# Kernel optimization log

Hardware: AMD Instinct MI355X
Metric: run time of the kernel (lower is better)

The kernel has to match this reference:

```python
import jax, jax.numpy as jnp
import numpy as np

NUM_HEADS = 16
MASKED_BIAS = -10000.0


def setup_inputs() -> dict:
    key = jax.random.key(0)
    k1, k2, k3 = jax.random.split(key, 3)
    B, S, D = 4, 2048, 1024
    scale = 0.02
    return {
        "hidden_states": jax.random.normal(k1, (B, S, D), dtype=jnp.float32),
        "c_attn_w": jax.random.normal(k2, (D, 3 * D), dtype=jnp.float32) * scale,
        "c_attn_b": jnp.zeros((3 * D,), dtype=jnp.float32),
        "c_proj_w": jax.random.normal(k3, (D, D), dtype=jnp.float32) * scale,
        "c_proj_b": jnp.zeros((D,), dtype=jnp.float32),
    }


def reference(hidden_states, c_attn_w, c_attn_b, c_proj_w, c_proj_b):
    B, S, D = hidden_states.shape
    H = NUM_HEADS
    hd = D // H
    # qkv projection (HF Conv1D: x @ W + b)
    qkv = hidden_states @ c_attn_w + c_attn_b  # [B, S, 3D]
    q, k, v = jnp.split(qkv, 3, axis=-1)

    def split_heads(t):
        return t.reshape(B, S, H, hd).transpose(0, 2, 1, 3)  # [B, H, S, hd]

    q, k, v = split_heads(q), split_heads(k), split_heads(v)
    # full score matrix [B, H, S, S] (eager attention)
    attn = jnp.einsum("bhqd,bhkd->bhqk", q, k) / jnp.sqrt(jnp.float32(hd))
    causal = jnp.tril(jnp.ones((S, S), dtype=bool))  # [S, S]
    attn = jnp.where(causal[None, None], attn, jnp.float32(MASKED_BIAS))
    attn = jax.nn.softmax(attn, axis=-1)
    out = jnp.einsum("bhqk,bhkd->bhqd", attn, v)  # [B, H, S, hd]
    out = out.transpose(0, 2, 1, 3).reshape(B, S, D)  # merge heads
    out = out @ c_proj_w + c_proj_b
    return out
```

## Files before the change

kernel.cpp:

```cpp
#include <hip/hip_runtime.h>

#define NH 16
#define HD 64

typedef __attribute__((ext_vector_type(8))) _Float16 f16x8;
typedef __attribute__((ext_vector_type(4))) float f32x4;
typedef __attribute__((ext_vector_type(8))) unsigned short us8;
typedef __attribute__((ext_vector_type(4))) unsigned short us4;
typedef __attribute__((ext_vector_type(2))) unsigned int u32x2;

#define CEXP 0.18033688f

__device__ __forceinline__ unsigned short f2h(float f) {
    _Float16 h = (_Float16)f;
    return __builtin_bit_cast(unsigned short, h);
}

__global__ __launch_bounds__(256)
void transpose_cast_both(const float* __restrict__ w1, unsigned short* __restrict__ o1,
                         const float* __restrict__ w2, unsigned short* __restrict__ o2) {
    __shared__ float T[64][65];
    const int R = 1024;
    int bx = blockIdx.x;
    const float* in; unsigned short* out; int C;
    if (bx < 48) { in = w1; out = o1; C = 3072; }
    else         { in = w2; out = o2; C = 1024; bx -= 48; }
    const int c0 = bx * 64, r0 = blockIdx.y * 64;
    const int tid = threadIdx.x;
    const int rr = tid >> 4, cc4 = (tid & 15) * 4;
    #pragma unroll
    for (int p = 0; p < 4; ++p) {
        int r = rr + p * 16;
        float4 v = *reinterpret_cast<const float4*>(
            in + (size_t)(r0 + r) * C + c0 + cc4);
        T[r][cc4] = v.x; T[r][cc4 + 1] = v.y; T[r][cc4 + 2] = v.z; T[r][cc4 + 3] = v.w;
    }
    __syncthreads();
    #pragma unroll
    for (int p = 0; p < 4; ++p) {
        int orow = rr + p * 16;
        us4 w;
        #pragma unroll
        for (int j = 0; j < 4; ++j) w[j] = f2h(T[cc4 + j][orow]);
        *reinterpret_cast<us4*>(out + (size_t)(c0 + orow) * R + r0 + cc4) = w;
    }
}

__device__ __forceinline__ void stage128(unsigned short* dst,
                                         const unsigned short* src, int stride) {
    const int tid = threadIdx.x;
    #pragma unroll
    for (int p = 0; p < 4; ++p) {
        int idx = tid + p * 256;
        int r = idx >> 3;
        int slot = idx & 7;
        us8 v = *reinterpret_cast<const us8*>(src + (size_t)r * stride + slot * 8);
        int cb = (slot << 4) ^ ((r & 7) << 4);
        *reinterpret_cast<us8*>(reinterpret_cast<char*>(dst) + r * 128 + cb) = v;
    }
}

__device__ __forceinline__ void stage128_f32(unsigned short* dst,
                                             const float* src, int stride) {
    const int tid = threadIdx.x;
    #pragma unroll
    for (int p = 0; p < 4; ++p) {
        int idx = tid + p * 256;
        int r = idx >> 3;
        int slot = idx & 7;
        const float* s = src + (size_t)r * stride + slot * 8;
        float4 a = *reinterpret_cast<const float4*>(s);
        float4 b = *reinterpret_cast<const float4*>(s + 4);
        uint4 w;
        w.x = __builtin_bit_cast(unsigned int, __builtin_amdgcn_cvt_pkrtz(a.x, a.y));
        w.y = __builtin_bit_cast(unsigned int, __builtin_amdgcn_cvt_pkrtz(a.z, a.w));
        w.z = __builtin_bit_cast(unsigned int, __builtin_amdgcn_cvt_pkrtz(b.x, b.y));
        w.w = __builtin_bit_cast(unsigned int, __builtin_amdgcn_cvt_pkrtz(b.z, b.w));
        int cb = (slot << 4) ^ ((r & 7) << 4);
        *reinterpret_cast<uint4*>(reinterpret_cast<char*>(dst) + r * 128 + cb) = w;
    }
}

__device__ __forceinline__ void stage64(unsigned short* dst,
                                        const unsigned short* src, int stride) {
    const int tid = threadIdx.x;
    #pragma unroll
    for (int p = 0; p < 2; ++p) {
        int idx = tid + p * 256;
        int r = idx >> 3;
        int slot = idx & 7;
        us8 v = *reinterpret_cast<const us8*>(src + (size_t)r * stride + slot * 8);
        int cb = (slot << 4) ^ ((r & 7) << 4);
        *reinterpret_cast<us8*>(reinterpret_cast<char*>(dst) + r * 128 + cb) = v;
    }
}

__device__ __forceinline__ f16x8 frag16(const unsigned short* base, int row0, int ks) {
    const int lane = threadIdx.x & 63;
    const int r = row0 + (lane & 15);
    int cb = ((ks << 6) + (lane & 48)) ^ ((r & 7) << 4);
    return *reinterpret_cast<const f16x8*>(
        reinterpret_cast<const char*>(base) + r * 128 + cb);
}

template<int MODE, int NX>
__global__ __launch_bounds__(256)
void gemm_f16(const void* __restrict__ Ax,
              const unsigned short* __restrict__ Bt,
              const float* __restrict__ bias,
              float* __restrict__ C,
              unsigned short* __restrict__ qb,
              unsigned short* __restrict__ kb,
              unsigned short* __restrict__ vtb,
              int M, int N, int K) {
    __shared__ __align__(16) unsigned short As[128 * 64];
    __shared__ __align__(16) unsigned short Bs[128 * 64];

    const int tid = threadIdx.x;
    const int wid = tid >> 6, lane = tid & 63, g = lane >> 4;
    const int wr = wid >> 1, wc = wid & 1;

    const int f = blockIdx.x;
    const int wi = f >> 3;
    const int m0 = ((wi / NX) * 8 + (f & 7)) * 128;
    const int n0 = (wi % NX) * 128;

    f32x4 acc[4][4];
    #pragma unroll
    for (int i = 0; i < 4; ++i)
        #pragma unroll
        for (int j = 0; j < 4; ++j) {
            acc[i][j][0] = 0.f; acc[i][j][1] = 0.f;
            acc[i][j][2] = 0.f; acc[i][j][3] = 0.f;
        }

    for (int k0 = 0; k0 < K; k0 += 64) {
        __syncthreads();
        if (MODE == 1)
            stage128_f32(As, (const float*)Ax + (size_t)m0 * K + k0, K);
        else
            stage128(As, (const unsigned short*)Ax + (size_t)m0 * K + k0, K);
        stage128(Bs, Bt + (size_t)n0 * K + k0, K);
        __syncthreads();

        f16x8 af[4][2], bf[4][2];
        #pragma unroll
        for (int mi = 0; mi < 4; ++mi)
            #pragma unroll
            for (int ks = 0; ks < 2; ++ks)
                af[mi][ks] = frag16(As, wr * 64 + mi * 16, ks);
        #pragma unroll
        for (int ni = 0; ni < 4; ++ni)
            #pragma unroll
            for (int ks = 0; ks < 2; ++ks)
                bf[ni][ks] = frag16(Bs, wc * 64 + ni * 16, ks);

        __builtin_amdgcn_s_setprio(1);
        #pragma unroll
        for (int ks = 0; ks < 2; ++ks)
            #pragma unroll
            for (int mi = 0; mi < 4; ++mi)
                #pragma unroll
                for (int ni = 0; ni < 4; ++ni)
                    acc[mi][ni] = __builtin_amdgcn_mfma_f32_16x16x32_f16(
                        af[mi][ks], bf[ni][ks], acc[mi][ni], 0, 0, 0);
        __builtin_amdgcn_s_setprio(0);
    }

    const int colBase = n0 + wc * 64;
    const int rowBase = m0 + wr * 64;

    if (MODE == 0) {
        #pragma unroll
        for (int ni = 0; ni < 4; ++ni) {
            int col = colBase + ni * 16 + (lane & 15);
            float bv = bias[col];
            #pragma unroll
            for (int mi = 0; mi < 4; ++mi) {
                int row = rowBase + mi * 16 + g * 4;
                #pragma unroll
                for (int reg = 0; reg < 4; ++reg)
                    C[(size_t)(row + reg) * N + col] = acc[mi][ni][reg] + bv;
            }
        }
    } else {
        #pragma unroll
        for (int ni = 0; ni < 4; ++ni) {
            int col = colBase + ni * 16 + (lane & 15);
            float bv = bias[col];
            int seg = col >> 10;
            int cc = col & 1023;
            int h = cc >> 6, d = cc & 63;
            const float sc = (seg == 0) ? CEXP : 1.0f;
            #pragma unroll
            for (int mi = 0; mi < 4; ++mi) {
                int row = rowBase + mi * 16 + g * 4;
                int b = row >> 11, s = row & 2047;
                size_t bh = (size_t)(b * NH + h);
                if (seg < 2) {
                    unsigned short* dst = (seg ? kb : qb)
                        + bh * 2048 * 64 + (size_t)s * 64 + d;
                    #pragma unroll
                    for (int reg = 0; reg < 4; ++reg)
                        dst[(size_t)reg * 64] = f2h((acc[mi][ni][reg] + bv) * sc);
                } else {
                    unsigned short* dst = vtb
                        + bh * 64 * 2048 + (size_t)d * 2048 + s;
                    us4 w;
                    #pragma unroll
                    for (int reg = 0; reg < 4; ++reg)
                        w[reg] = f2h(acc[mi][ni][reg] + bv);
                    *reinterpret_cast<us4*>(dst) = w;
                }
            }
        }
    }
}

template<bool DIAG>
__device__ __forceinline__ void attn_tile(
    f16x8 qf0, f16x8 qf1,
    const unsigned short* Ks, const unsigned short* Vs, unsigned short* Pw,
    f32x4 (&o)[4], float& l_,
    int kt, int qrow_base, int lane, int g) {

    f32x4 s[4];
    #pragma unroll
    for (int n = 0; n < 4; ++n) { s[n][0] = 0.f; s[n][1] = 0.f; s[n][2] = 0.f; s[n][3] = 0.f; }

    __builtin_amdgcn_s_setprio(1);
    #pragma unroll
    for (int ks = 0; ks < 2; ++ks) {
        f16x8 b = ks ? qf1 : qf0;
        #pragma unroll
        for (int n = 0; n < 4; ++n)
            s[n] = __builtin_amdgcn_mfma_f32_16x16x32_f16(
                frag16(Ks, n * 16, ks), b, s[n], 0, 0, 0);
    }
    __builtin_amdgcn_s_setprio(0);

    const int q = lane & 15;
    float psum = 0.f;
    #pragma unroll
    for (int n = 0; n < 4; ++n) {
        float p0 = __builtin_exp2f(s[n][0]);
        float p1 = __builtin_exp2f(s[n][1]);
        float p2 = __builtin_exp2f(s[n][2]);
        float p3 = __builtin_exp2f(s[n][3]);
        if (DIAG) {
            const int kb_ = kt * 64 + (g << 2) + 16 * n;
            const int qg = qrow_base + q;
            p0 = (kb_ + 0 > qg) ? 0.f : p0;
            p1 = (kb_ + 1 > qg) ? 0.f : p1;
            p2 = (kb_ + 2 > qg) ? 0.f : p2;
            p3 = (kb_ + 3 > qg) ? 0.f : p3;
        }
        psum += (p0 + p1) + (p2 + p3);
        u32x2 w;
        w[0] = __builtin_bit_cast(unsigned int, __builtin_amdgcn_cvt_pkrtz(p0, p1));
        w[1] = __builtin_bit_cast(unsigned int, __builtin_amdgcn_cvt_pkrtz(p2, p3));
        int pcb = ((n << 5) + (g << 3)) ^ ((q & 7) << 4);
        *reinterpret_cast<u32x2*>(
            reinterpret_cast<char*>(Pw) + q * 128 + pcb) = w;
    }
    l_ += psum;

    __builtin_amdgcn_s_setprio(1);
    #pragma unroll
    for (int ks = 0; ks < 2; ++ks) {
        f16x8 pa = frag16(Pw, 0, ks);
        #pragma unroll
        for (int n = 0; n < 4; ++n)
            o[n] = __builtin_amdgcn_mfma_f32_16x16x32_f16(
                pa, frag16(Vs, n * 16, ks), o[n], 0, 0, 0);
    }
    __builtin_amdgcn_s_setprio(0);
}

__global__ __launch_bounds__(256, 4)
void attn_mfma(const unsigned short* __restrict__ qb,
               const unsigned short* __restrict__ kb,
               const unsigned short* __restrict__ vtb,
               unsigned short* __restrict__ attno) {
    const int f = blockIdx.x;
    const int xcd = f & 7;
    const int wi = f >> 3;
    const int bh = xcd * 8 + (wi >> 4);
    const int pair = wi & 15;
    const int qtA = pair, qtB = 31 - pair;
    const int tid = threadIdx.x;
    const int wid = tid >> 6, lane = tid & 63, g = lane >> 4;

    __shared__ __align__(16) unsigned short Ks[64 * 64];
    __shared__ __align__(16) unsigned short Vs[64 * 64];
    __shared__ __align__(16) unsigned short Ps[4][16 * 64];

    const unsigned short* kg0 = kb + (size_t)bh * 2048 * 64;
    const unsigned short* vg0 = vtb + (size_t)bh * 64 * 2048;

    const int qrl = wid * 16 + (lane & 15);
    const int qd0 = (lane >> 4) * 8;
    const unsigned short* qbase = qb + (size_t)bh * 2048 * 64;
    f16x8 qA0 = *reinterpret_cast<const f16x8*>(qbase + (size_t)(qtA * 64 + qrl) * 64 + qd0);
    f16x8 qA1 = *reinterpret_cast<const f16x8*>(qbase + (size_t)(qtA * 64 + qrl) * 64 + 32 + qd0);
    f16x8 qB0 = *reinterpret_cast<const f16x8*>(qbase + (size_t)(qtB * 64 + qrl) * 64 + qd0);
    f16x8 qB1 = *reinterpret_cast<const f16x8*>(qbase + (size_t)(qtB * 64 + qrl) * 64 + 32 + qd0);

    f32x4 oA[4], oB[4];
    float lA = 0.f, lB = 0.f;
    #pragma unroll
    for (int n = 0; n < 4; ++n) {
        #pragma unroll
        for (int r = 0; r < 4; ++r) { oA[n][r] = 0.f; oB[n][r] = 0.f; }
    }

    unsigned short* Pw = Ps[wid];
    const int qrbA = qtA * 64 + wid * 16;
    const int qrbB = qtB * 64 + wid * 16;

    auto STAGE = [&](int kt) {
        __syncthreads();
        stage64(Ks, kg0 + (size_t)kt * 64 * 64, 64);
        stage64(Vs, vg0 + (size_t)kt * 64, 2048);
        __syncthreads();
    };

    for (int kt = 0; kt < qtA; ++kt) {
        STAGE(kt);
        attn_tile<false>(qB0, qB1, Ks, Vs, Pw, oB, lB, kt, qrbB, lane, g);
        attn_tile<false>(qA0, qA1, Ks, Vs, Pw, oA, lA, kt, qrbA, lane, g);
    }
    STAGE(qtA);
    attn_tile<false>(qB0, qB1, Ks, Vs, Pw, oB, lB, qtA, qrbB, lane, g);
    attn_tile<true >(qA0, qA1, Ks, Vs, Pw, oA, lA, qtA, qrbA, lane, g);
    for (int kt = qtA + 1; kt < qtB; ++kt) {
        STAGE(kt);
        attn_tile<false>(qB0, qB1, Ks, Vs, Pw, oB, lB, kt, qrbB, lane, g);
    }
    STAGE(qtB);
    attn_tile<true >(qB0, qB1, Ks, Vs, Pw, oB, lB, qtB, qrbB, lane, g);

    const int b = bh >> 4, h = bh & 15;
    #pragma unroll
    for (int ph = 0; ph < 2; ++ph) {
        const int qt = ph ? qtB : qtA;
        f32x4* o = ph ? oB : oA;
        float ltot = ph ? lB : lA;
        ltot += __shfl_xor(ltot, 16);
        ltot += __shfl_xor(ltot, 32);
        unsigned short* ob = attno
            + (size_t)(b * 2048 + qt * 64 + wid * 16) * 1024 + h * 64;
        #pragma unroll
        for (int reg = 0; reg < 4; ++reg) {
            int row = (g << 2) + reg;
            float inv = 1.0f / __shfl(ltot, row);
            #pragma unroll
            for (int n = 0; n < 4; ++n)
                ob[(size_t)row * 1024 + n * 16 + (lane & 15)] = f2h(o[n][reg] * inv);
        }
    }
}

extern "C" void kernel_launch(void* const* d_in, const int* in_sizes, int n_in,
                              void* d_out, int out_size, void* d_ws, size_t ws_size,
                              hipStream_t stream) {
    const float* x    = (const float*)d_in[0];
    const float* Wqkv = (const float*)d_in[1];
    const float* bqkv = (const float*)d_in[2];
    const float* Wp   = (const float*)d_in[3];
    const float* bp   = (const float*)d_in[4];
    float* out = (float*)d_out;

    const int B = 4, S = 2048, D = 1024;
    const int M = B * S;
    const size_t HSZ = (size_t)M * D;

    unsigned short* wqt   = (unsigned short*)d_ws;
    unsigned short* wpt   = wqt + (size_t)3 * D * D;
    unsigned short* qbuf  = wpt + (size_t)D * D;
    unsigned short* kbuf  = qbuf + HSZ;
    unsigned short* vtb   = kbuf + HSZ;
    unsigned short* attno = vtb + HSZ;

    dim3 blk(256);
    transpose_cast_both<<<dim3(64, 16), blk, 0, stream>>>(Wqkv, wqt, Wp, wpt);

    gemm_f16<1, 24><<<dim3(1536), blk, 0, stream>>>(
        x, wqt, bqkv, nullptr, qbuf, kbuf, vtb, M, 3 * D, D);
    attn_mfma<<<dim3(1024), blk, 0, stream>>>(qbuf, kbuf, vtb, attno);
    gemm_f16<0, 8><<<dim3(512), blk, 0, stream>>>(
        attno, wpt, bp, out, nullptr, nullptr, nullptr, M, D, D);
}
```

Before: 173.8 us.

## Switch attention to 32x32x16 MFMA with 128-row query chunks per block

Reworks the attention kernel so each wave handles 32 query rows with 32x32x16 MFMA tiles instead of 16-row 16x16x32 tiles. Each block now processes two 128-row query chunks paired for causal load balance, halving the grid and the number of K/V stage loads per query row. The aim is to raise K/V reuse per shared-memory stage and MFMA efficiency. The cost is larger per-thread accumulators and lower occupancy (launch bound 2), plus more wasted work in the diagonal tiles.

```diff
diff --git a/kernel.cpp b/kernel.cpp
--- a/kernel.cpp
+++ b/kernel.cpp
@@ -5,6 +5,7 @@
 
 typedef __attribute__((ext_vector_type(8))) _Float16 f16x8;
 typedef __attribute__((ext_vector_type(4))) float f32x4;
+typedef __attribute__((ext_vector_type(16))) float f32x16;
 typedef __attribute__((ext_vector_type(8))) unsigned short us8;
 typedef __attribute__((ext_vector_type(4))) unsigned short us4;
 typedef __attribute__((ext_vector_type(2))) unsigned int u32x2;
@@ -99,6 +100,14 @@
     const int lane = threadIdx.x & 63;
     const int r = row0 + (lane & 15);
     int cb = ((ks << 6) + (lane & 48)) ^ ((r & 7) << 4);
+    return *reinterpret_cast<const f16x8*>(
+        reinterpret_cast<const char*>(base) + r * 128 + cb);
+}
+
+__device__ __forceinline__ f16x8 frag32(const unsigned short* base, int row0, int c) {
+    const int lane = threadIdx.x & 63;
+    const int r = row0 + (lane & 31);
+    int cb = ((c << 5) + ((lane >> 5) << 4)) ^ ((r & 7) << 4);
     return *reinterpret_cast<const f16x8*>(
         reinterpret_cast<const char*>(base) + r * 128 + cb);
 }
@@ -218,66 +227,69 @@
 }
 
 template<bool DIAG>
-__device__ __forceinline__ void attn_tile(
-    f16x8 qf0, f16x8 qf1,
+__device__ __forceinline__ void attn_slice(
+    const f16x8 (&qf)[4],
     const unsigned short* Ks, const unsigned short* Vs, unsigned short* Pw,
-    f32x4 (&o)[4], float& l_,
-    int kt, int qrow_base, int lane, int g) {
-
-    f32x4 s[4];
-    #pragma unroll
-    for (int n = 0; n < 4; ++n) { s[n][0] = 0.f; s[n][1] = 0.f; s[n][2] = 0.f; s[n][3] = 0.f; }
+    f32x16 (&o)[2], float& l_, int kt, int qsb, int lane) {
+
+    const int hf = lane >> 5;
+    const int q = lane & 31;
+
+    f32x16 s[2];
+    #pragma unroll
+    for (int n = 0; n < 2; ++n)
+        #pragma unroll
+        for (int r = 0; r < 16; ++r) s[n][r] = 0.f;
 
     __builtin_amdgcn_s_setprio(1);
     #pragma unroll
-    for (int ks = 0; ks < 2; ++ks) {
-        f16x8 b = ks ? qf1 : qf0;
-        #pragma unroll
-        for (int n = 0; n < 4; ++n)
-            s[n] = __builtin_amdgcn_mfma_f32_16x16x32_f16(
-                frag16(Ks, n * 16, ks), b, s[n], 0, 0, 0);
+    for (int c = 0; c < 4; ++c) {
+        #pragma unroll
+        for (int n = 0; n < 2; ++n)
+            s[n] = __builtin_amdgcn_mfma_f32_32x32x16_f16(
+                frag32(Ks, n * 32, c), qf[c], s[n], 0, 0, 0);
     }
     __builtin_amdgcn_s_setprio(0);
 
-    const int q = lane & 15;
+    const int qg = qsb + q;
     float psum = 0.f;
     #pragma unroll
-    for (int n = 0; n < 4; ++n) {
-        float p0 = __builtin_exp2f(s[n][0]);
-        float p1 = __builtin_exp2f(s[n][1]);
-        float p2 = __builtin_exp2f(s[n][2]);
-        float p3 = __builtin_exp2f(s[n][3]);
-        if (DIAG) {
-            const int kb_ = kt * 64 + (g << 2) + 16 * n;
-            const int qg = qrow_base + q;
-            p0 = (kb_ + 0 > qg) ? 0.f : p0;
-            p1 = (kb_ + 1 > qg) ? 0.f : p1;
-            p2 = (kb_ + 2 > qg) ? 0.f : p2;
-            p3 = (kb_ + 3 > qg) ? 0.f : p3;
+    for (int n = 0; n < 2; ++n) {
+        #pragma unroll
+        for (int j = 0; j < 4; ++j) {
+            float p[4];
+            #pragma unroll
+            for (int i = 0; i < 4; ++i) {
+                float v = __builtin_exp2f(s[n][j * 4 + i]);
+                if (DIAG) {
+                    int kg = kt * 64 + n * 32 + 8 * j + 4 * hf + i;
+                    if (kg > qg) v = 0.f;
+                }
+                p[i] = v; psum += v;
+            }
+            u32x2 w;
+            w[0] = __builtin_bit_cast(unsigned int, __builtin_amdgcn_cvt_pkrtz(p[0], p[1]));
+            w[1] = __builtin_bit_cast(unsigned int, __builtin_amdgcn_cvt_pkrtz(p[2], p[3]));
+            int pb = (n * 64 + j * 16 + hf * 8) ^ ((q & 7) << 4);
+            *reinterpret_cast<u32x2*>(
+                reinterpret_cast<char*>(Pw) + q * 128 + pb) = w;
         }
-        psum += (p0 + p1) + (p2 + p3);
-        u32x2 w;
-        w[0] = __builtin_bit_cast(unsigned int, __builtin_amdgcn_cvt_pkrtz(p0, p1));
-        w[1] = __builtin_bit_cast(unsigned int, __builtin_amdgcn_cvt_pkrtz(p2, p3));
-        int pcb = ((n << 5) + (g << 3)) ^ ((q & 7) << 4);
-        *reinterpret_cast<u32x2*>(
-            reinterpret_cast<char*>(Pw) + q * 128 + pcb) = w;
     }
     l_ += psum;
 
     __builtin_amdgcn_s_setprio(1);
     #pragma unroll
-    for (int ks = 0; ks < 2; ++ks) {
-        f16x8 pa = frag16(Pw, 0, ks);
-        #pragma unroll
-        for (int n = 0; n < 4; ++n)
-            o[n] = __builtin_amdgcn_mfma_f32_16x16x32_f16(
-                pa, frag16(Vs, n * 16, ks), o[n], 0, 0, 0);
+    for (int c = 0; c < 4; ++c) {
+        f16x8 pf = frag32(Pw, 0, c);
+        #pragma unroll
+        for (int n2 = 0; n2 < 2; ++n2)
+            o[n2] = __builtin_amdgcn_mfma_f32_32x32x16_f16(
+                pf, frag32(Vs, n2 * 32, c), o[n2], 0, 0, 0);
     }
     __builtin_amdgcn_s_setprio(0);
 }
 
-__global__ __launch_bounds__(256, 4)
+__global__ __launch_bounds__(256, 2)
 void attn_mfma(const unsigned short* __restrict__ qb,
                const unsigned short* __restrict__ kb,
                const unsigned short* __restrict__ vtb,
@@ -285,78 +297,78 @@
     const int f = blockIdx.x;
     const int xcd = f & 7;
     const int wi = f >> 3;
-    const int bh = xcd * 8 + (wi >> 4);
-    const int pair = wi & 15;
-    const int qtA = pair, qtB = 31 - pair;
-    const int tid = threadIdx.x;
-    const int wid = tid >> 6, lane = tid & 63, g = lane >> 4;
+    const int bh = xcd * 8 + (wi >> 3);
+    const int t = wi & 7;
+    const int cA = t, cB = 15 - t;
+    const int tid = threadIdx.x;
+    const int wid = tid >> 6, lane = tid & 63;
 
     __shared__ __align__(16) unsigned short Ks[64 * 64];
     __shared__ __align__(16) unsigned short Vs[64 * 64];
-    __shared__ __align__(16) unsigned short Ps[4][16 * 64];
+    __shared__ __align__(16) unsigned short Ps[4][32 * 64];
 
     const unsigned short* kg0 = kb + (size_t)bh * 2048 * 64;
     const unsigned short* vg0 = vtb + (size_t)bh * 64 * 2048;
 
-    const int qrl = wid * 16 + (lane & 15);
-    const int qd0 = (lane >> 4) * 8;
+    const int qsbA = cA * 128 + wid * 32;
+    const int qsbB = cB * 128 + wid * 32;
+    const int mA = qsbA >> 6, mB = qsbB >> 6;
+
     const unsigned short* qbase = qb + (size_t)bh * 2048 * 64;
-    f16x8 qA0 = *reinterpret_cast<const f16x8*>(qbase + (size_t)(qtA * 64 + qrl) * 64 + qd0);
-    f16x8 qA1 = *reinterpret_cast<const f16x8*>(qbase + (size_t)(qtA * 64 + qrl) * 64 + 32 + qd0);
-    f16x8 qB0 = *reinterpret_cast<const f16x8*>(qbase + (size_t)(qtB * 64 + qrl) * 64 + qd0);
-    f16x8 qB1 = *reinterpret_cast<const f16x8*>(qbase + (size_t)(qtB * 64 + qrl) * 64 + 32 + qd0);
-
-    f32x4 oA[4], oB[4];
+    const int qoff = ((lane >> 5) << 4);
+    f16x8 qfA[4], qfB[4];
+    #pragma unroll
+    for (int c = 0; c < 4; ++c) {
+        qfA[c] = *reinterpret_cast<const f16x8*>(
+            reinterpret_cast<const char*>(qbase + (size_t)(qsbA + (lane & 31)) * 64)
+            + c * 32 + qoff);
+        qfB[c] = *reinterpret_cast<const f16x8*>(
+            reinterpret_cast<const char*>(qbase + (size_t)(qsbB + (lane & 31)) * 64)
+            + c * 32 + qoff);
+    }
+
+    f32x16 oA[2], oB[2];
+    #pragma unroll
+    for (int n = 0; n < 2; ++n)
+        #pragma unroll
+        for (int r = 0; r < 16; ++r) { oA[n][r] = 0.f; oB[n][r] = 0.f; }
     float lA = 0.f, lB = 0.f;
-    #pragma unroll
-    for (int n = 0; n < 4; ++n) {
-        #pragma unroll
-        for (int r = 0; r < 4; ++r) { oA[n][r] = 0.f; oB[n][r] = 0.f; }
-    }
 
     unsigned short* Pw = Ps[wid];
-    const int qrbA = qtA * 64 + wid * 16;
-    const int qrbB = qtB * 64 + wid * 16;
-
-    auto STAGE = [&](int kt) {
+    const int kmax = 2 * cB + 1;
+
+    for (int kt = 0; kt <= kmax; ++kt) {
         __syncthreads();
         stage64(Ks, kg0 + (size_t)kt * 64 * 64, 64);
         stage64(Vs, vg0 + (size_t)kt * 64, 2048);
         __syncthreads();
-    };
-
-    for (int kt = 0; kt < qtA; ++kt) {
-        STAGE(kt);
-        attn_tile<false>(qB0, qB1, Ks, Vs, Pw, oB, lB, kt, qrbB, lane, g);
-        attn_tile<false>(qA0, qA1, Ks, Vs, Pw, oA, lA, kt, qrbA, lane, g);
-    }
-    STAGE(qtA);
-    attn_tile<false>(qB0, qB1, Ks, Vs, Pw, oB, lB, qtA, qrbB, lane, g);
-    attn_tile<true >(qA0, qA1, Ks, Vs, Pw, oA, lA, qtA, qrbA, lane, g);
-    for (int kt = qtA + 1; kt < qtB; ++kt) {
-        STAGE(kt);
-        attn_tile<false>(qB0, qB1, Ks, Vs, Pw, oB, lB, kt, qrbB, lane, g);
-    }
-    STAGE(qtB);
-    attn_tile<true >(qB0, qB1, Ks, Vs, Pw, oB, lB, qtB, qrbB, lane, g);
-
-    const int b = bh >> 4, h = bh & 15;
+
+        if (kt < mB)       attn_slice<false>(qfB, Ks, Vs, Pw, oB, lB, kt, qsbB, lane);
+        else if (kt == mB) attn_slice<true >(qfB, Ks, Vs, Pw, oB, lB, kt, qsbB, lane);
+        if (kt < mA)       attn_slice<false>(qfA, Ks, Vs, Pw, oA, lA, kt, qsbA, lane);
+        else if (kt == mA) attn_slice<true >(qfA, Ks, Vs, Pw, oA, lA, kt, qsbA, lane);
+    }
+
+    const int b = bh >> 4, hh = bh & 15;
+    const int hf = lane >> 5;
     #pragma unroll
     for (int ph = 0; ph < 2; ++ph) {
-        const int qt = ph ? qtB : qtA;
-        f32x4* o = ph ? oB : oA;
+        const int qsb = ph ? qsbB : qsbA;
+        f32x16* o = ph ? oB : oA;
         float ltot = ph ? lB : lA;
-        ltot += __shfl_xor(ltot, 16);
         ltot += __shfl_xor(ltot, 32);
         unsigned short* ob = attno
-            + (size_t)(b * 2048 + qt * 64 + wid * 16) * 1024 + h * 64;
-        #pragma unroll
-        for (int reg = 0; reg < 4; ++reg) {
-            int row = (g << 2) + reg;
-            float inv = 1.0f / __shfl(ltot, row);
-            #pragma unroll
-            for (int n = 0; n < 4; ++n)
-                ob[(size_t)row * 1024 + n * 16 + (lane & 15)] = f2h(o[n][reg] * inv);
+            + (size_t)(b * 2048 + qsb) * 1024 + hh * 64 + (lane & 31);
+        #pragma unroll
+        for (int n2 = 0; n2 < 2; ++n2) {
+            #pragma unroll
+            for (int j = 0; j < 4; ++j)
+                #pragma unroll
+                for (int i = 0; i < 4; ++i) {
+                    int qloc = i + 8 * j + 4 * hf;
+                    float inv = 1.0f / __shfl(ltot, qloc);
+                    ob[(size_t)qloc * 1024 + n2 * 32] = f2h(o[n2][j * 4 + i] * inv);
+                }
         }
     }
 }
@@ -387,7 +399,7 @@
 
     gemm_f16<1, 24><<<dim3(1536), blk, 0, stream>>>(
         x, wqt, bqkv, nullptr, qbuf, kbuf, vtb, M, 3 * D, D);
-    attn_mfma<<<dim3(1024), blk, 0, stream>>>(qbuf, kbuf, vtb, attno);
+    attn_mfma<<<dim3(512), blk, 0, stream>>>(qbuf, kbuf, vtb, attno);
     gemm_f16<0, 8><<<dim3(512), blk, 0, stream>>>(
         attno, wpt, bp, out, nullptr, nullptr, nullptr, M, D, D);
 }
```

New measurement: 174.8 us. About the same (+0.6%).
